# Kernel optimization log

Hardware: AMD Instinct MI355X
Metric: run time of the kernel (lower is better)

## Reference

```python
import jax, jax.numpy as jnp
import numpy as np

# Module constants (match init_kwargs / torch defaults)
NUM_HEADS = 8
A, B_COEF, C_COEF = 0.5, 1.0, 1.0
EPS = 1e-12  # torch F.normalize eps


def _l2_normalize(x):
    n = jnp.maximum(jnp.linalg.norm(x, axis=-1, keepdims=True), EPS)
    return x / n


def setup_inputs() -> dict:
    key = jax.random.key(0)
    ks = jax.random.split(key, 4)
    Bb, N, C = 1, 4096, 384
    x = jax.random.normal(ks[0], (Bb, N, C), dtype=jnp.float32)
    qkv_w = jax.random.normal(ks[1], (3 * C, C), dtype=jnp.float32) * 0.02
    qkv_b = jnp.zeros((3 * C,), dtype=jnp.float32)
    proj_w = jax.random.normal(ks[2], (C, C), dtype=jnp.float32) * 0.02
    proj_b = jnp.zeros((C,), dtype=jnp.float32)
    temperature = jnp.ones((1, NUM_HEADS, 1, 1), dtype=jnp.float32)
    return {"x": x, "qkv_w": qkv_w, "qkv_b": qkv_b, "proj_w": proj_w,
            "proj_b": proj_b, "temperature": temperature}


def reference(x, qkv_w, qkv_b, proj_w, proj_b, temperature):
    Bb, N, C = x.shape
    H = NUM_HEADS
    d = C // H
    scale = d ** 0.25

    qkv = x @ qkv_w.T + qkv_b                       # (B, N, 3C)
    qkv = qkv.reshape(Bb, N, 3, H, d).transpose(2, 0, 3, 1, 4)  # (3, B, H, N, d)
    q, k, v = qkv[0], qkv[1], qkv[2]
    q = q * (C ** -0.5)

    # efficient attention (N > N0 = d^2 + d + 1)
    v1 = jnp.concatenate([jnp.ones((Bb, H, N, 1), dtype=v.dtype), v], axis=-1)  # (B,H,N,d+1)
    # normalize_input=True path
    q = _l2_normalize(q) * (scale * temperature)
    k = _l2_normalize(k) * scale
    v1 = v1 / N

    # kv_mod = box(k,k)^T @ v1  ->  (B, H, d, d, d+1)
    kv_mod = jnp.einsum('bhni,bhnj,bhnf->bhijf', k, k, v1)
    # quadratic term: a * box(q,q) @ kv_mod
    y = A * jnp.einsum('bhni,bhnj,bhijf->bhnf', q, q, kv_mod)
    # linear term: scale^2 * b * q @ (k^T @ v1)
    kv = jnp.einsum('bhnd,bhnf->bhdf', k, v1)
    y = y + (scale ** 2) * B_COEF * jnp.einsum('bhnd,bhdf->bhnf', q, kv)
    # constant term: scale^4 * c * sum_n v1
    y = y + (scale ** 4) * C_COEF * jnp.sum(v1, axis=-2, keepdims=True)

    y_norm, y_out = y[..., :1], y[..., 1:]
    out = y_out / y_norm                             # (B, H, N, d)

    out = out.transpose(0, 2, 1, 3).reshape(Bb, N, C)
    out = out @ proj_w.T + proj_b
    return out
```

## Files before the change

kernel.cpp:

```cpp
#include <hip/hip_runtime.h>

#define HN 8
#define NN 4096
#define CC 384
#define DD 48
#define DP 64
#define NPAIR 1225
#define PPAD 1280
#define MPF 52

typedef unsigned short ushort;
typedef unsigned int uint;
typedef __attribute__((ext_vector_type(8))) short short8;
typedef __attribute__((ext_vector_type(4))) float f32x4;

__device__ __forceinline__ float4 ld4(const float* p){ return *reinterpret_cast<const float4*>(p); }
__device__ __forceinline__ void st4(float* p, const float4& v){ *reinterpret_cast<float4*>(p) = v; }

__device__ __forceinline__ uint bf16rtn(float x){
  uint u = __float_as_uint(x);
  return (u + 0x7FFFu + ((u >> 16) & 1u)) >> 16;
}

__global__ __launch_bounds__(256) void split_f32(const float* __restrict__ in,
                                                 ushort* __restrict__ hi,
                                                 ushort* __restrict__ lo,
                                                 int n4) {
  int idx = blockIdx.x * 256 + threadIdx.x;
  if (idx >= n4) return;
  float4 v = ld4(in + (size_t)idx * 4);
  float bv[4] = {v.x, v.y, v.z, v.w};
  uint hu[2], lu[2];
#pragma unroll
  for (int e = 0; e < 2; ++e) {
    float x0 = bv[2*e], x1 = bv[2*e+1];
    uint h0 = bf16rtn(x0), h1 = bf16rtn(x1);
    float d0 = x0 - __uint_as_float(h0 << 16);
    float d1 = x1 - __uint_as_float(h1 << 16);
    hu[e] = h0 | (h1 << 16);
    lu[e] = (__float_as_uint(d0) >> 16) | (__float_as_uint(d1) & 0xFFFF0000u);
  }
  *reinterpret_cast<uint2*>(hi + (size_t)idx*4) = make_uint2(hu[0], hu[1]);
  *reinterpret_cast<uint2*>(lo + (size_t)idx*4) = make_uint2(lu[0], lu[1]);
}

#define GST 40
__global__ __launch_bounds__(256) void gemm_bf16(const ushort* __restrict__ Ah,
                                                 const ushort* __restrict__ Al,
                                                 const float*  __restrict__ Bw,
                                                 const float*  __restrict__ bias,
                                                 float* __restrict__ Cm,
                                                 int M, int Nc, int K) {
  __shared__ ushort AsH[2][128*GST], AsL[2][128*GST];
  __shared__ ushort BsH[2][64*GST],  BsL[2][64*GST];
  const int tid = threadIdx.x;
  const int n0 = blockIdx.x * 64;
  const int m0 = blockIdx.y * 128;
  const int lane = tid & 63, wv = tid >> 6;
  const int wr = wv >> 1, wc = wv & 1;
  const int lr = lane & 15, lg = lane >> 4;
  const int ar = tid >> 1, ap = (tid & 1) << 4;
  const int br = tid >> 2, bp = (tid & 3) << 3;
  const ushort* gAh = Ah + (size_t)(m0 + ar) * K + ap;
  const ushort* gAl = Al + (size_t)(m0 + ar) * K + ap;
  const float*  gB  = Bw + (size_t)(n0 + br) * K + bp;
  uint4 rah0, rah1, ral0, ral1;
  float4 rb0, rb1;
#define G_LOAD(T) { int kk = (T)*32; \
    rah0 = *reinterpret_cast<const uint4*>(gAh + kk); \
    rah1 = *reinterpret_cast<const uint4*>(gAh + kk + 8); \
    ral0 = *reinterpret_cast<const uint4*>(gAl + kk); \
    ral1 = *reinterpret_cast<const uint4*>(gAl + kk + 8); \
    rb0 = ld4(gB + kk); rb1 = ld4(gB + kk + 4); }
#define G_WRITE(BUF) { \
    *reinterpret_cast<uint4*>(&AsH[BUF][ar*GST+ap])   = rah0; \
    *reinterpret_cast<uint4*>(&AsH[BUF][ar*GST+ap+8]) = rah1; \
    *reinterpret_cast<uint4*>(&AsL[BUF][ar*GST+ap])   = ral0; \
    *reinterpret_cast<uint4*>(&AsL[BUF][ar*GST+ap+8]) = ral1; \
    float bv[8] = {rb0.x,rb0.y,rb0.z,rb0.w,rb1.x,rb1.y,rb1.z,rb1.w}; \
    uint hu[4], lu[4]; \
    _Pragma("unroll") for (int e = 0; e < 4; ++e) { \
      float x0 = bv[2*e], x1 = bv[2*e+1]; \
      uint h0 = bf16rtn(x0), h1 = bf16rtn(x1); \
      float d0 = x0 - __uint_as_float(h0 << 16); \
      float d1 = x1 - __uint_as_float(h1 << 16); \
      hu[e] = h0 | (h1 << 16); \
      lu[e] = (__float_as_uint(d0) >> 16) | (__float_as_uint(d1) & 0xFFFF0000u); } \
    *reinterpret_cast<uint4*>(&BsH[BUF][br*GST+bp]) = make_uint4(hu[0],hu[1],hu[2],hu[3]); \
    *reinterpret_cast<uint4*>(&BsL[BUF][br*GST+bp]) = make_uint4(lu[0],lu[1],lu[2],lu[3]); }

  f32x4 acc[4][2];
#pragma unroll
  for (int pf = 0; pf < 4; ++pf)
#pragma unroll
    for (int ff = 0; ff < 2; ++ff) acc[pf][ff] = (f32x4)0.f;

  G_LOAD(0);
  G_WRITE(0);
  G_LOAD(1);
  const int NT = K / 32;
  int cur = 0;
  __syncthreads();
  for (int t = 0; t < NT; ++t) {
    short8 a_h[4], a_l[4], b_h[2], b_l[2];
#pragma unroll
    for (int pf = 0; pf < 4; ++pf) {
      int row = wr*64 + pf*16 + lr;
      a_h[pf] = *reinterpret_cast<const short8*>(&AsH[cur][row*GST + lg*8]);
      a_l[pf] = *reinterpret_cast<const short8*>(&AsL[cur][row*GST + lg*8]);
    }
#pragma unroll
    for (int ff = 0; ff < 2; ++ff) {
      int col = wc*32 + ff*16 + lr;
      b_h[ff] = *reinterpret_cast<const short8*>(&BsH[cur][col*GST + lg*8]);
      b_l[ff] = *reinterpret_cast<const short8*>(&BsL[cur][col*GST + lg*8]);
    }
    if (t < NT-1) { G_WRITE(cur^1); }
    if (t < NT-2) { G_LOAD(t+2); }
#pragma unroll
    for (int pf = 0; pf < 4; ++pf)
#pragma unroll
      for (int ff = 0; ff < 2; ++ff) {
        acc[pf][ff] = __builtin_amdgcn_mfma_f32_16x16x32_bf16(a_h[pf], b_h[ff], acc[pf][ff], 0, 0, 0);
        acc[pf][ff] = __builtin_amdgcn_mfma_f32_16x16x32_bf16(a_h[pf], b_l[ff], acc[pf][ff], 0, 0, 0);
        acc[pf][ff] = __builtin_amdgcn_mfma_f32_16x16x32_bf16(a_l[pf], b_h[ff], acc[pf][ff], 0, 0, 0);
      }
    __syncthreads();
    cur ^= 1;
  }
#pragma unroll
  for (int pf = 0; pf < 4; ++pf)
#pragma unroll
    for (int ff = 0; ff < 2; ++ff) {
      int col = n0 + wc*32 + ff*16 + lr;
      float bs = bias[col];
#pragma unroll
      for (int reg = 0; reg < 4; ++reg) {
        int row = m0 + wr*64 + pf*16 + lg*4 + reg;
        Cm[(size_t)row*Nc + col] = acc[pf][ff][reg] + bs;
      }
    }
#undef G_LOAD
#undef G_WRITE
}

__global__ __launch_bounds__(256) void prep2(const float* __restrict__ qkv,
                                             const float* __restrict__ temperature,
                                             float* __restrict__ Qb,
                                             float* __restrict__ KbT,
                                             ushort* __restrict__ VhT,
                                             ushort* __restrict__ VlT) {
  __shared__ float Ks[64*65];
  __shared__ float Vs[64*65];
  const int nb = blockIdx.x;
  const int h  = blockIdx.y;
  const int lane = threadIdx.x & 63;
  const int w = threadIdx.x >> 6;
  const float temp = temperature[h];
  const float CINV = 0.05103103630798288f;
  const float S4   = 2.6321480259049848f;
  for (int r = 0; r < 16; ++r) {
    const int nl = w*16 + r;
    const int n  = nb*64 + nl;
    const float* row = qkv + (size_t)n * (3*CC) + h * DD;
    float qv = (lane < DD) ? row[lane] : 0.f;
    float kv = (lane < DD) ? row[CC + lane] : 0.f;
    float vv = (lane >= 1 && lane <= DD) ? row[2*CC + lane - 1] : 0.f;
    float qs = qv * CINV;
    float q2 = qs * qs;
    float k2 = kv * kv;
#pragma unroll
    for (int off = 32; off > 0; off >>= 1) {
      q2 += __shfl_xor(q2, off);
      k2 += __shfl_xor(k2, off);
    }
    float qn = qs / fmaxf(sqrtf(q2), 1e-12f) * (S4 * temp);
    float kn = kv / fmaxf(sqrtf(k2), 1e-12f) * S4;
    float qo = (lane < DD) ? qn : ((lane == DD) ? 6.928203230275509f : 0.f);
    float ko = (lane < DD) ? kn : ((lane == DD) ? 1.f : 0.f);
    float vo = (lane == 0) ? (1.f/NN) : ((lane <= DD) ? vv * (1.f/NN) : 0.f);
    Qb[((size_t)h * NN + n) * DP + lane] = qo;
    Ks[nl*65 + lane] = ko;
    Vs[nl*65 + lane] = vo;
  }
  __syncthreads();
  const int ch = threadIdx.x >> 2;
  const int q4 = threadIdx.x & 3;
  float kc[16], vc[16];
#pragma unroll
  for (int e = 0; e < 16; ++e) {
    int nl = q4*16 + e;
    kc[e] = Ks[nl*65 + ch];
    vc[e] = Vs[nl*65 + ch];
  }
  size_t tbase = ((size_t)h*64 + ch) * NN + nb*64 + q4*16;
#pragma unroll
  for (int e = 0; e < 16; e += 4)
    st4(KbT + tbase + e, make_float4(kc[e], kc[e+1], kc[e+2], kc[e+3]));
  uint hu[8], lu[8];
#pragma unroll
  for (int e = 0; e < 8; ++e) {
    float v0 = vc[2*e], v1 = vc[2*e+1];
    uint h0 = bf16rtn(v0), h1 = bf16rtn(v1);
    float d0 = v0 - __uint_as_float(h0 << 16);
    float d1 = v1 - __uint_as_float(h1 << 16);
    uint t0 = __float_as_uint(d0), t1 = __float_as_uint(d1);
    hu[e] = h0 | (h1 << 16);
    lu[e] = (t0 >> 16) | (t1 & 0xFFFF0000u);
  }
  *reinterpret_cast<uint4*>(VhT + tbase)     = make_uint4(hu[0],hu[1],hu[2],hu[3]);
  *reinterpret_cast<uint4*>(VhT + tbase + 8) = make_uint4(hu[4],hu[5],hu[6],hu[7]);
  *reinterpret_cast<uint4*>(VlT + tbase)     = make_uint4(lu[0],lu[1],lu[2],lu[3]);
  *reinterpret_cast<uint4*>(VlT + tbase + 8) = make_uint4(lu[4],lu[5],lu[6],lu[7]);
}

#define KST 40
#define KNST 36
__global__ __launch_bounds__(256) void kvmod_mfma(const float* __restrict__ KbT,
                                                  const ushort* __restrict__ VhT,
                                                  const ushort* __restrict__ VlT,
                                                  float* __restrict__ Mp) {
  __shared__ ushort KKh[256*KST];
  __shared__ ushort KKl[256*KST];
  __shared__ float  KnS[64*KNST];
  __shared__ ushort VhS[64*KST];
  __shared__ ushort VlS[64*KST];
  const int tid  = threadIdx.x;
  const int bid  = blockIdx.x;
  const int h    = bid & 7;
  const int idx  = bid >> 3;
  const int p0   = (idx % 5) * 256;
  const int part = idx / 5;
  const int nbase = part * 512;
  int ii = 63, jj = 63;
  {
    int pg = p0 + tid;
    if (pg < NPAIR) {
      int i = 0, rem = pg;
      while (rem >= 49 - i) { rem -= 49 - i; ++i; }
      ii = i; jj = i + rem;
    }
  }
  const float* krow_i = &KnS[ii*KNST];
  const float* krow_j = &KnS[jj*KNST];
  const int sch = tid >> 2;
  const int sq  = tid & 3;
  const size_t kgbase = ((size_t)h*64 + sch) * NN + nbase;
  const int lane = tid & 63, wv = tid >> 6;
  const int lr = lane & 15, lg = lane >> 4;
  f32x4 acc[4][4];
#pragma unroll
  for (int a = 0; a < 4; ++a)
#pragma unroll
    for (int b = 0; b < 4; ++b) acc[a][b] = (f32x4)0.f;

  for (int t = 0; t < 16; ++t) {
    const int k0 = t * 32;
    __syncthreads();
    {
      float4 a0 = ld4(KbT + kgbase + k0 + sq*8);
      float4 a1 = ld4(KbT + kgbase + k0 + sq*8 + 4);
      st4(&KnS[sch*KNST + sq*8], a0);
      st4(&KnS[sch*KNST + sq*8 + 4], a1);
      *reinterpret_cast<uint4*>(&VhS[sch*KST + sq*8]) =
          *reinterpret_cast<const uint4*>(VhT + kgbase + k0 + sq*8);
      *reinterpret_cast<uint4*>(&VlS[sch*KST + sq*8]) =
          *reinterpret_cast<const uint4*>(VlT + kgbase + k0 + sq*8);
    }
    __syncthreads();
    {
      uint hu[16], lu[16];
#pragma unroll
      for (int g = 0; g < 8; ++g) {
        float4 a = ld4(krow_i + g*4);
        float4 b = ld4(krow_j + g*4);
        float m0 = a.x*b.x, m1 = a.y*b.y, m2 = a.z*b.z, m3 = a.w*b.w;
        uint h0 = bf16rtn(m0), h1 = bf16rtn(m1), h2 = bf16rtn(m2), h3 = bf16rtn(m3);
        float d0 = m0 - __uint_as_float(h0 << 16);
        float d1 = m1 - __uint_as_float(h1 << 16);
        float d2 = m2 - __uint_as_float(h2 << 16);
        float d3 = m3 - __uint_as_float(h3 << 16);
        uint t0 = __float_as_uint(d0), t1 = __float_as_uint(d1);
        uint t2 = __float_as_uint(d2), t3 = __float_as_uint(d3);
        hu[2*g]   = h0 | (h1 << 16);
        hu[2*g+1] = h2 | (h3 << 16);
        lu[2*g]   = (t0 >> 16) | (t1 & 0xFFFF0000u);
        lu[2*g+1] = (t2 >> 16) | (t3 & 0xFFFF0000u);
      }
      uint4* dh = reinterpret_cast<uint4*>(&KKh[tid*KST]);
      uint4* dl = reinterpret_cast<uint4*>(&KKl[tid*KST]);
      dh[0] = make_uint4(hu[0],hu[1],hu[2],hu[3]);
      dh[1] = make_uint4(hu[4],hu[5],hu[6],hu[7]);
      dh[2] = make_uint4(hu[8],hu[9],hu[10],hu[11]);
      dh[3] = make_uint4(hu[12],hu[13],hu[14],hu[15]);
      dl[0] = make_uint4(lu[0],lu[1],lu[2],lu[3]);
      dl[1] = make_uint4(lu[4],lu[5],lu[6],lu[7]);
      dl[2] = make_uint4(lu[8],lu[9],lu[10],lu[11]);
      dl[3] = make_uint4(lu[12],lu[13],lu[14],lu[15]);
    }
    __syncthreads();
    short8 ah[4], al[4], bh[4], bl[4];
#pragma unroll
    for (int pf = 0; pf < 4; ++pf) {
      int prow = wv*64 + pf*16 + lr;
      ah[pf] = *reinterpret_cast<const short8*>(&KKh[prow*KST + lg*8]);
      al[pf] = *reinterpret_cast<const short8*>(&KKl[prow*KST + lg*8]);
    }
#pragma unroll
    for (int ff = 0; ff < 4; ++ff) {
      int frow = ff*16 + lr;
      bh[ff] = *reinterpret_cast<const short8*>(&VhS[frow*KST + lg*8]);
      bl[ff] = *reinterpret_cast<const short8*>(&VlS[frow*KST + lg*8]);
    }
#pragma unroll
    for (int pf = 0; pf < 4; ++pf)
#pragma unroll
      for (int ff = 0; ff < 4; ++ff) {
        acc[pf][ff] = __builtin_amdgcn_mfma_f32_16x16x32_bf16(ah[pf], bh[ff], acc[pf][ff], 0, 0, 0);
        acc[pf][ff] = __builtin_amdgcn_mfma_f32_16x16x32_bf16(ah[pf], bl[ff], acc[pf][ff], 0, 0, 0);
        acc[pf][ff] = __builtin_amdgcn_mfma_f32_16x16x32_bf16(al[pf], bh[ff], acc[pf][ff], 0, 0, 0);
      }
  }
  float* out = Mp + ((size_t)(part*HN + h) * PPAD + p0 + wv*64) * MPF;
#pragma unroll
  for (int pf = 0; pf < 4; ++pf)
#pragma unroll
    for (int ff = 0; ff < 4; ++ff) {
      int f = ff*16 + lr;
      if (f < MPF) {
#pragma unroll
        for (int reg = 0; reg < 4; ++reg) {
          int prow = pf*16 + lg*4 + reg;
          out[prow*MPF + f] = acc[pf][ff][reg];
        }
      }
    }
}

__global__ __launch_bounds__(256) void reduce_mirror(const float* __restrict__ Mp,
                                                     ushort* __restrict__ Mbh,
                                                     ushort* __restrict__ Mbl,
                                                     float* __restrict__ Mnorm) {
  const int pb = blockIdx.x;
  const int h  = blockIdx.y;
  const int pl = threadIdx.x & 63;
  const int fq0 = threadIdx.x >> 6;
  const int p = pb*64 + pl;
  if (p >= NPAIR) return;
  int i = 0, rem = p;
  while (rem >= 49 - i) { rem -= 49 - i; ++i; }
  const int j = i + rem;
  for (int fq = fq0; fq < 13; fq += 4) {
    float4 s = make_float4(0.f, 0.f, 0.f, 0.f);
#pragma unroll
    for (int part = 0; part < 8; ++part) {
      float4 a = ld4(Mp + ((size_t)(part*HN + h) * PPAD + p) * MPF + fq*4);
      s.x += a.x; s.y += a.y; s.z += a.z; s.w += a.w;
    }
    float sv[4] = {s.x, s.y, s.z, s.w};
#pragma unroll
    for (int c = 0; c < 4; ++c) {
      int f = fq*4 + c;
      float v = sv[c];
      uint hb = bf16rtn(v);
      float d = v - __uint_as_float(hb << 16);
      ushort lb = (ushort)(__float_as_uint(d) >> 16);
      size_t a1 = (((size_t)h*49 + i)*64 + f)*64 + j;
      size_t a2 = (((size_t)h*49 + j)*64 + f)*64 + i;
      Mbh[a1] = (ushort)hb; Mbl[a1] = lb;
      Mbh[a2] = (ushort)hb; Mbl[a2] = lb;
    }
    if (p == NPAIR-1) st4(&Mnorm[h*64 + fq*4], s);
  }
}

__global__ __launch_bounds__(256, 3) void y_mfma(const float* __restrict__ Qb,
                                                 const ushort* __restrict__ Mbh,
                                                 const ushort* __restrict__ Mbl,
                                                 float* __restrict__ Yp) {
  __shared__ float QT[28*128];
  __shared__ ushort Mt[2][2][32*64];
  const int tid = threadIdx.x;
  const int bid = blockIdx.x;
  const int h   = bid & 7;
  const int rest = bid >> 3;
  const int n0  = (rest & 31) * 128;
  const int z   = rest >> 5;
  const int zi = z >> 1;
  const int zf = z & 1;
  const int ibase = zi * 25;
  const int ni = zi ? 24 : 25;
  const int lane = tid & 63;
  const int wv = tid >> 6;
  const int lr = lane & 15, lg = lane >> 4;

  {
    const int ng = (ni + 3) >> 2;
    for (int v = tid; v < ng*128; v += 256) {
      int r = v & 127;
      int cg = v >> 7;
      float4 q = ld4(Qb + ((size_t)h*NN + n0 + r)*DP + ibase + cg*4);
      QT[(cg*4+0)*128 + r] = q.x;
      QT[(cg*4+1)*128 + r] = q.y;
      QT[(cg*4+2)*128 + r] = q.z;
      QT[(cg*4+3)*128 + r] = q.w;
    }
  }
  short8 ah[2][2], al[2][2];
#pragma unroll
  for (int m = 0; m < 2; ++m) {
    const float* qr = Qb + ((size_t)h*NN + n0 + wv*32 + m*16 + lr)*DP + lg*8;
#pragma unroll
    for (int kc = 0; kc < 2; ++kc) {
      float4 v0 = ld4(qr + kc*32);
      float4 v1 = ld4(qr + kc*32 + 4);
      float qv[8] = {v0.x,v0.y,v0.z,v0.w,v1.x,v1.y,v1.z,v1.w};
      union { uint u[4]; short8 s; } chh, cll;
#pragma unroll
      for (int e = 0; e < 4; ++e) {
        float x0 = qv[2*e], x1 = qv[2*e+1];
        uint h0 = bf16rtn(x0), h1 = bf16rtn(x1);
        float d0 = x0 - __uint_as_float(h0 << 16);
        float d1 = x1 - __uint_as_float(h1 << 16);
        chh.u[e] = h0 | (h1 << 16);
        cll.u[e] = (__float_as_uint(d0) >> 16) | (__float_as_uint(d1) & 0xFFFF0000u);
      }
      ah[m][kc] = chh.s;
      al[m][kc] = cll.s;
    }
  }
  const int sp   = tid >> 7;
  const int ss   = tid & 127;
  const int srow = ss >> 2;
  const int sc2  = (ss & 3) * 2;
  const ushort* gsrc = (sp ? Mbl : Mbh) + (size_t)h*49*4096 + (zf*32 + srow)*64 + sc2*8;
  uint4 pre[2];
#define Y_LOAD(I) { const uint4* gp = reinterpret_cast<const uint4*>(gsrc + (size_t)(I)*4096); \
    pre[0] = gp[0]; pre[1] = gp[1]; }
#define Y_WRITE(BUF) { _Pragma("unroll") for (int e = 0; e < 2; ++e) { \
    int slot = (sc2 + e) ^ (srow & 7); \
    *reinterpret_cast<uint4*>(&Mt[BUF][sp][srow*64 + slot*8]) = pre[e]; } }

  Y_LOAD(ibase);
  Y_WRITE(0);
  Y_LOAD(ibase+1);

  f32x4 ya[2][2];
#pragma unroll
  for (int m = 0; m < 2; ++m)
#pragma unroll
    for (int ff = 0; ff < 2; ++ff) ya[m][ff] = (f32x4)0.f;

  int cur = 0;
  __syncthreads();
  for (int li = 0; li < ni; ++li) {
    short8 bh[2][2], bl[2][2];
#pragma unroll
    for (int kc = 0; kc < 2; ++kc)
#pragma unroll
      for (int ff = 0; ff < 2; ++ff) {
        int row = ff*16 + lr;
        int slot = (kc*4 + lg) ^ (row & 7);
        bh[kc][ff] = *reinterpret_cast<const short8*>(&Mt[cur][0][row*64 + slot*8]);
        bl[kc][ff] = *reinterpret_cast<const short8*>(&Mt[cur][1][row*64 + slot*8]);
      }
    if (li < ni-1) { Y_WRITE(cur^1); }
    if (li < ni-2) { Y_LOAD(ibase+li+2); }
#pragma unroll
    for (int m = 0; m < 2; ++m) {
      float4 qi = ld4(&QT[li*128 + wv*32 + m*16 + lg*4]);
#pragma unroll
      for (int ff = 0; ff < 2; ++ff) {
        f32x4 acc = (f32x4)0.f;
        acc = __builtin_amdgcn_mfma_f32_16x16x32_bf16(ah[m][0], bh[0][ff], acc, 0, 0, 0);
        acc = __builtin_amdgcn_mfma_f32_16x16x32_bf16(ah[m][0], bl[0][ff], acc, 0, 0, 0);
        acc = __builtin_amdgcn_mfma_f32_16x16x32_bf16(al[m][0], bh[0][ff], acc, 0, 0, 0);
        acc = __builtin_amdgcn_mfma_f32_16x16x32_bf16(ah[m][1], bh[1][ff], acc, 0, 0, 0);
        acc = __builtin_amdgcn_mfma_f32_16x16x32_bf16(ah[m][1], bl[1][ff], acc, 0, 0, 0);
        acc = __builtin_amdgcn_mfma_f32_16x16x32_bf16(al[m][1], bh[1][ff], acc, 0, 0, 0);
        ya[m][ff][0] += qi.x * acc[0];
        ya[m][ff][1] += qi.y * acc[1];
        ya[m][ff][2] += qi.z * acc[2];
        ya[m][ff][3] += qi.w * acc[3];
      }
    }
    __syncthreads();
    cur ^= 1;
  }
  float* out = Yp + ((size_t)(zi*HN + h) * NN) * 64;
#pragma unroll
  for (int m = 0; m < 2; ++m)
#pragma unroll
    for (int ff = 0; ff < 2; ++ff) {
      int f = zf*32 + ff*16 + lr;
#pragma unroll
      for (int reg = 0; reg < 4; ++reg) {
        int row = n0 + wv*32 + m*16 + lg*4 + reg;
        out[(size_t)row*64 + f] = ya[m][ff][reg];
      }
    }
#undef Y_LOAD
#undef Y_WRITE
}

__global__ __launch_bounds__(256) void y_combine(const float* __restrict__ Yp,
                                                 const float* __restrict__ Mnorm,
                                                 ushort* __restrict__ AttnH,
                                                 ushort* __restrict__ AttnL) {
  const int h = blockIdx.y;
  const int t = threadIdx.x;
  const int r = blockIdx.x*64 + (t >> 2);
  const int fq = t & 3;
  const int lane = t & 63;
  const float* p0 = Yp + ((size_t)h*NN + r)*64 + fq*16;
  const float* p1 = Yp + ((size_t)(HN+h)*NN + r)*64 + fq*16;
  float y[16];
#pragma unroll
  for (int g = 0; g < 4; ++g) {
    float4 a = ld4(p0 + g*4);
    float4 b = ld4(p1 + g*4);
    float4 m = ld4(Mnorm + h*64 + fq*16 + g*4);
    y[g*4+0] = 0.5f*(a.x+b.x) + 24.f*m.x;
    y[g*4+1] = 0.5f*(a.y+b.y) + 24.f*m.y;
    y[g*4+2] = 0.5f*(a.z+b.z) + 24.f*m.z;
    y[g*4+3] = 0.5f*(a.w+b.w) + 24.f*m.w;
  }
  float y0 = __shfl(y[0], lane & ~3);
  float inv = 1.f / y0;
#pragma unroll
  for (int e = 0; e < 16; ++e) {
    int f = fq*16 + e;
    if (f >= 1 && f <= DD) {
      float o = y[e] * inv;
      uint hb = bf16rtn(o);
      float d = o - __uint_as_float(hb << 16);
      size_t a = (size_t)r*CC + h*DD + (f-1);
      AttnH[a] = (ushort)hb;
      AttnL[a] = (ushort)(__float_as_uint(d) >> 16);
    }
  }
}

extern "C" void kernel_launch(void* const* d_in, const int* in_sizes, int n_in,
                              void* d_out, int out_size, void* d_ws, size_t ws_size,
                              hipStream_t stream) {
  const float* x      = (const float*)d_in[0];
  const float* qkv_w  = (const float*)d_in[1];
  const float* qkv_b  = (const float*)d_in[2];
  const float* proj_w = (const float*)d_in[3];
  const float* proj_b = (const float*)d_in[4];
  const float* temp   = (const float*)d_in[5];
  float* ws = (float*)d_ws;

  float*  qkv  = ws;
  float*  Mp   = ws;
  float*  Yp   = ws;
  float*  Qb   = ws + 4718592;
  ushort* Xh   = (ushort*)(ws + 6815744);
  ushort* Xl   = Xh + 1572864;
  float*  KbT  = ws + 6815744;
  ushort* Mbh  = (ushort*)(ws + 6815744);
  ushort* Mbl  = Mbh + 1605632;
  float*  Mnorm= ws + 6815744 + 1605632;
  ushort* VhT  = (ushort*)(ws + 8912896);
  ushort* VlT  = (ushort*)(ws + 9961472);
  ushort* AttnH= (ushort*)(ws + 8912896);
  ushort* AttnL= AttnH + 1572864;

  split_f32<<<1536, 256, 0, stream>>>(x, Xh, Xl, NN*CC/4);
  {
    dim3 g(1152/64, 4096/128);
    gemm_bf16<<<g, 256, 0, stream>>>(Xh, Xl, qkv_w, qkv_b, qkv, 4096, 1152, 384);
  }
  {
    dim3 g(64, HN);
    prep2<<<g, 256, 0, stream>>>(qkv, temp, Qb, KbT, VhT, VlT);
  }
  kvmod_mfma<<<320, 256, 0, stream>>>(KbT, VhT, VlT, Mp);
  hipMemsetAsync((void*)Mbh, 0, 2*(size_t)1605632*2 + 2048, stream);
  {
    dim3 g(PPAD/64, HN);
    reduce_mirror<<<g, 256, 0, stream>>>(Mp, Mbh, Mbl, Mnorm);
  }
  y_mfma<<<1024, 256, 0, stream>>>(Qb, Mbh, Mbl, Yp);
  {
    dim3 g(4096/64, HN);
    y_combine<<<g, 256, 0, stream>>>(Yp, Mnorm, AttnH, AttnL);
  }
  {
    dim3 g(384/64, 4096/128);
    gemm_bf16<<<g, 256, 0, stream>>>(AttnH, AttnL, proj_w, proj_b, (float*)d_out, 4096, 384, 384);
  }
}
```

Before: 203.0 us.

## Use raw LDS-only barriers and prefetch next K/V tile in kv_mod kernel

Replaces __syncthreads with an inline-asm barrier that waits only on LDS counters (lgkmcnt), so global prefetch loads stay in flight across barriers in the GEMM, kv_mod and y kernels. In the kv_mod kernel it adds register prefetch of the next K/V tile, issued right after staging the current tile, so global latency overlaps the product and MFMA work. The risks are that the raw barrier skips waiting on vmcnt, and that correctness relies on the compiler inserting waits before the registers are used. The asm memory clobber may also limit scheduling.

```diff
diff --git a/kernel.cpp b/kernel.cpp
--- a/kernel.cpp
+++ b/kernel.cpp
@@ -16,6 +16,8 @@
 
 __device__ __forceinline__ float4 ld4(const float* p){ return *reinterpret_cast<const float4*>(p); }
 __device__ __forceinline__ void st4(float* p, const float4& v){ *reinterpret_cast<float4*>(p) = v; }
+
+#define RAW_BAR() asm volatile("s_waitcnt lgkmcnt(0)\ns_barrier" ::: "memory")
 
 __device__ __forceinline__ uint bf16rtn(float x){
   uint u = __float_as_uint(x);
@@ -100,7 +102,7 @@
   G_LOAD(1);
   const int NT = K / 32;
   int cur = 0;
-  __syncthreads();
+  RAW_BAR();
   for (int t = 0; t < NT; ++t) {
     short8 a_h[4], a_l[4], b_h[2], b_l[2];
 #pragma unroll
@@ -125,7 +127,7 @@
         acc[pf][ff] = __builtin_amdgcn_mfma_f32_16x16x32_bf16(a_h[pf], b_l[ff], acc[pf][ff], 0, 0, 0);
         acc[pf][ff] = __builtin_amdgcn_mfma_f32_16x16x32_bf16(a_l[pf], b_h[ff], acc[pf][ff], 0, 0, 0);
       }
-    __syncthreads();
+    RAW_BAR();
     cur ^= 1;
   }
 #pragma unroll
@@ -254,20 +256,24 @@
 #pragma unroll
     for (int b = 0; b < 4; ++b) acc[a][b] = (f32x4)0.f;
 
+  float4 pa0, pa1; uint4 pvh, pvl;
+#define PRE_LOAD(T) { int k0_ = (T)*32; \
+    pa0 = ld4(KbT + kgbase + k0_ + sq*8); \
+    pa1 = ld4(KbT + kgbase + k0_ + sq*8 + 4); \
+    pvh = *reinterpret_cast<const uint4*>(VhT + kgbase + k0_ + sq*8); \
+    pvl = *reinterpret_cast<const uint4*>(VlT + kgbase + k0_ + sq*8); }
+#define STAGE_WRITE() { \
+    st4(&KnS[sch*KNST + sq*8], pa0); \
+    st4(&KnS[sch*KNST + sq*8 + 4], pa1); \
+    *reinterpret_cast<uint4*>(&VhS[sch*KST + sq*8]) = pvh; \
+    *reinterpret_cast<uint4*>(&VlS[sch*KST + sq*8]) = pvl; }
+
+  PRE_LOAD(0);
   for (int t = 0; t < 16; ++t) {
-    const int k0 = t * 32;
-    __syncthreads();
-    {
-      float4 a0 = ld4(KbT + kgbase + k0 + sq*8);
-      float4 a1 = ld4(KbT + kgbase + k0 + sq*8 + 4);
-      st4(&KnS[sch*KNST + sq*8], a0);
-      st4(&KnS[sch*KNST + sq*8 + 4], a1);
-      *reinterpret_cast<uint4*>(&VhS[sch*KST + sq*8]) =
-          *reinterpret_cast<const uint4*>(VhT + kgbase + k0 + sq*8);
-      *reinterpret_cast<uint4*>(&VlS[sch*KST + sq*8]) =
-          *reinterpret_cast<const uint4*>(VlT + kgbase + k0 + sq*8);
-    }
-    __syncthreads();
+    RAW_BAR();
+    STAGE_WRITE();
+    if (t < 15) { PRE_LOAD(t+1); }
+    RAW_BAR();
     {
       uint hu[16], lu[16];
 #pragma unroll
@@ -298,7 +304,7 @@
       dl[2] = make_uint4(lu[8],lu[9],lu[10],lu[11]);
       dl[3] = make_uint4(lu[12],lu[13],lu[14],lu[15]);
     }
-    __syncthreads();
+    RAW_BAR();
     short8 ah[4], al[4], bh[4], bl[4];
 #pragma unroll
     for (int pf = 0; pf < 4; ++pf) {
@@ -335,6 +341,8 @@
         }
       }
     }
+#undef PRE_LOAD
+#undef STAGE_WRITE
 }
 
 __global__ __launch_bounds__(256) void reduce_mirror(const float* __restrict__ Mp,
@@ -452,7 +460,7 @@
     for (int ff = 0; ff < 2; ++ff) ya[m][ff] = (f32x4)0.f;
 
   int cur = 0;
-  __syncthreads();
+  RAW_BAR();
   for (int li = 0; li < ni; ++li) {
     short8 bh[2][2], bl[2][2];
 #pragma unroll
@@ -484,7 +492,7 @@
         ya[m][ff][3] += qi.w * acc[3];
       }
     }
-    __syncthreads();
+    RAW_BAR();
     cur ^= 1;
   }
   float* out = Yp + ((size_t)(zi*HN + h) * NN) * 64;
```

Result: no change. 201.4 us (-0.8%).
